# Performance work log

Measured on AMD Instinct MI355X. Metric: run time of the kernel, lower is better.

## Reference

```python
import jax, jax.numpy as jnp
import numpy as np

B, NPG, D, E = 64, 1024, 128, 524288
N = B * NPG
K1, K2, K3 = 820, 656, 525  # ceil(0.8*1024), ceil(0.8*820), ceil(0.8*656)
VOCAB = 100000
EPS = 1e-5


def setup_inputs() -> dict:
    key = jax.random.key(0)
    ks = jax.random.split(key, 16)
    epg = E // B
    off = jnp.repeat(jnp.arange(B, dtype=jnp.int32) * NPG, epg)
    src = jax.random.randint(ks[0], (E,), 0, NPG, dtype=jnp.int32) + off
    dst = jax.random.randint(ks[1], (E,), 0, NPG, dtype=jnp.int32) + off
    edge_index = jnp.stack([src, dst])  # [2, E], within-graph edges
    node_idx = jax.random.randint(ks[2], (N, 1), 0, VOCAB, dtype=jnp.int32)
    def lin(k, o, i):
        return jax.random.normal(k, (o, i), jnp.float32) / np.sqrt(i).astype(np.float32)
    return dict(
        node_idx=node_idx, edge_index=edge_index,
        emb=jax.random.normal(ks[3], (VOCAB, D), jnp.float32),
        w1l=lin(ks[4], 128, D), b1l=jnp.zeros(128, jnp.float32), w1r=lin(ks[5], 128, D),
        pool_w=jax.random.normal(ks[6], (128,), jnp.float32) / np.float32(np.sqrt(128)),
        w2l=lin(ks[7], 128, 128), b2l=jnp.zeros(128, jnp.float32), w2r=lin(ks[8], 128, 128),
        fc1_w=lin(ks[9], 128, 256), fc1_b=jnp.zeros(128, jnp.float32),
        bn1_g=jnp.ones(128, jnp.float32), bn1_b=jnp.zeros(128, jnp.float32),
        fc2_w=lin(ks[10], 64, 128), fc2_b=jnp.zeros(64, jnp.float32),
        bn2_g=jnp.ones(64, jnp.float32), bn2_b=jnp.zeros(64, jnp.float32),
        lin_w=lin(ks[11], 1, 64), lin_b=jnp.zeros(1, jnp.float32),
    )


def _sage(x, src, dst, em, wl, bl, wr):
    # PyG SAGEConv: lin_l(mean_{j->i} x_j) + lin_r(x_i); em masks dropped edges
    n = x.shape[0]
    s = jax.ops.segment_sum(x[src] * em[:, None], dst, num_segments=n)
    c = jax.ops.segment_sum(em, dst, num_segments=n)
    mean = s / jnp.maximum(c, 1.0)[:, None]
    return mean @ wl.T + bl + x @ wr.T


def _topk(x, src, dst, em, w, k):
    # PyG TopKPooling: score = x.w/||w||, per-graph top-k, gate by tanh(score)
    n = x.shape[0]
    npg = n // B
    score = (x @ w) / jnp.linalg.norm(w)
    vals, idx = jax.lax.top_k(score.reshape(B, npg), k)  # [B,k]
    perm = (idx + (jnp.arange(B, dtype=idx.dtype) * npg)[:, None]).reshape(-1)
    xn = x[perm] * jnp.tanh(vals).reshape(-1)[:, None]
    new_id = jnp.full((n,), -1, jnp.int32).at[perm].set(jnp.arange(B * k, dtype=jnp.int32))
    ns, nd = new_id[src], new_id[dst]
    em2 = em * (ns >= 0) * (nd >= 0)  # keep only edges with both endpoints kept
    return xn, jnp.maximum(ns, 0), jnp.maximum(nd, 0), em2


def _readout(x, k):
    # global_max_pool || global_mean_pool (graphs are contiguous, size k)
    xr = x.reshape(B, k, -1)
    return jnp.concatenate([xr.max(axis=1), xr.mean(axis=1)], axis=1)


def _bn(x, g, b):
    m = x.mean(0)
    v = jnp.mean((x - m) ** 2, axis=0)  # biased var, as in BatchNorm1d training
    return (x - m) / jnp.sqrt(v + EPS) * g + b


def reference(node_idx, edge_index, emb, w1l, b1l, w1r, pool_w,
              w2l, b2l, w2r, fc1_w, fc1_b, bn1_g, bn1_b,
              fc2_w, fc2_b, bn2_g, bn2_b, lin_w, lin_b):
    src, dst = edge_index[0], edge_index[1]
    em = jnp.ones((E,), jnp.float32)
    x = emb[node_idx[:, 0]]                                   # [N,128]
    x = jax.nn.relu(_sage(x, src, dst, em, w1l, b1l, w1r))
    x, src, dst, em = _topk(x, src, dst, em, pool_w, K1)
    x1 = _readout(x, K1)
    x = jax.nn.relu(_sage(x, src, dst, em, w2l, b2l, w2r))
    x, src, dst, em = _topk(x, src, dst, em, pool_w, K2)
    x2 = _readout(x, K2)
    x = jax.nn.relu(_sage(x, src, dst, em, w2l, b2l, w2r))
    x, src, dst, em = _topk(x, src, dst, em, pool_w, K3)
    x3 = _readout(x, K3)
    h = x1 + x2 + x3                                          # [B,256]
    h = jax.nn.relu(_bn(h @ fc1_w.T + fc1_b, bn1_g, bn1_b))
    h = jax.nn.relu(_bn(h @ fc2_w.T + fc2_b, bn2_g, bn2_b))
    # dropout is identity in eval mode
    return jax.nn.sigmoid(h @ lin_w.T + lin_b)[:, 0]          # [B]
```

## Files before the change

### kernel.cpp

```cpp
#include <hip/hip_runtime.h>
#include <hip/hip_bf16.h>
#include <cstdint>
#include <cstddef>

#define NGRAPH 64
#define NPG0   1024
#define NNODE  65536
#define NEDGE  524288
#define EPG    8192
#define DIM    128
#define RCHUNK 16

typedef __attribute__((ext_vector_type(8))) short short8v;
typedef __attribute__((ext_vector_type(4))) float f32x4;

__device__ __forceinline__ unsigned bf16rne(float f) {
  unsigned u = __float_as_uint(f);
  return (u + 0x7FFFu + ((u >> 16) & 1u)) >> 16;
}

__global__ __launch_bounds__(256) void k_gather(const float* __restrict__ emb,
    const int* __restrict__ nid, float* __restrict__ x)
{
  int tid = blockIdx.x * 256 + threadIdx.x;
  int i = tid >> 5, lane = tid & 31;
  int row = nid[i];
  ((float4*)(x + (size_t)i * DIM))[lane] =
      ((const float4*)(emb + (size_t)row * DIM))[lane];
}

__global__ __launch_bounds__(64) void k_norm(const float* __restrict__ pw,
    float* __restrict__ inv_norm)
{
  int t = threadIdx.x;
  float a = pw[t], b = pw[t + 64];
  float v = a * a + b * b;
  for (int off = 32; off; off >>= 1) v += __shfl_xor(v, off);
  if (t == 0) *inv_norm = 1.0f / sqrtf(v);
}

__global__ __launch_bounds__(256) void k_prep_wfrag(
    const float* __restrict__ w1l, const float* __restrict__ w1r,
    const float* __restrict__ w2l, const float* __restrict__ w2r,
    short* __restrict__ whiF, short* __restrict__ wloF)
{
  int id = blockIdx.x * 256 + threadIdx.x;
  int set = id >> 15;
  int r = id & 32767;
  int j  = r & 7;
  int l  = (r >> 3) & 63;
  int nt = (r >> 9) & 7;
  int kk = r >> 12;
  int k = kk * 32 + ((l >> 4) & 3) * 8 + j;
  int n = nt * 16 + (l & 15);
  const float* wl = set ? w2l : w1l;
  const float* wr = set ? w2r : w1r;
  float w = (k < 128) ? wl[n * 128 + k] : wr[n * 128 + (k - 128)];
  unsigned hb = bf16rne(w);
  float hif = __uint_as_float(hb << 16);
  unsigned lb = bf16rne(w - hif);
  whiF[id] = (short)hb;
  wloF[id] = (short)lb;
}

__global__ __launch_bounds__(1024) void k_csr0(const int* __restrict__ ei,
    int* __restrict__ off_g, int* __restrict__ elist_g, float* __restrict__ c_out)
{
  __shared__ int cnt[1024];
  __shared__ int cur[1024];
  __shared__ int wsum[16];
  const int t = threadIdx.x, g = blockIdx.x;
  const int nodeBase = g * NPG0;
  const int e0 = g * EPG;
  cnt[t] = 0;
  __syncthreads();
  int sv8[8], dl8[8];
  #pragma unroll
  for (int i = 0; i < 8; ++i) {
    int e = e0 + t + i * 1024;
    sv8[i] = ei[e];
    dl8[i] = ei[NEDGE + e] - nodeBase;
    atomicAdd(&cnt[dl8[i]], 1);
  }
  __syncthreads();
  const int lane = t & 63, w = t >> 6;
  int cv = cnt[t];
  int x = cv;
  #pragma unroll
  for (int off = 1; off < 64; off <<= 1) {
    int y = __shfl_up(x, off);
    if (lane >= off) x += y;
  }
  if (lane == 63) wsum[w] = x;
  __syncthreads();
  if (t < 16) {
    int v = wsum[t];
    #pragma unroll
    for (int off2 = 1; off2 < 16; off2 <<= 1) {
      int y = __shfl_up(v, off2);
      if (t >= off2) v += y;
    }
    wsum[t] = v;
  }
  __syncthreads();
  int incl = x + (w ? wsum[w - 1] : 0);
  int excl = incl - cv;
  cur[t] = excl;
  int* offp = off_g + g * 1025;
  offp[t] = excl;
  if (t == 1023) offp[1024] = incl;
  c_out[nodeBase + t] = (float)cv;
  __syncthreads();
  int* elp = elist_g + g * EPG;
  #pragma unroll
  for (int i = 0; i < 8; ++i) {
    int pos = atomicAdd(&cur[dl8[i]], 1);
    elp[pos] = sv8[i];
  }
}

__global__ __launch_bounds__(256) void k_gather_agg(
    const int* __restrict__ off_g, const int* __restrict__ elist_g,
    const float* __restrict__ x, float* __restrict__ s_out, int npg)
{
  const int g  = blockIdx.x & 63;
  const int sb = blockIdx.x >> 6;
  const int t = threadIdx.x;
  const int gr = t >> 5;
  const int l32 = t & 31;
  const int nq16 = (npg + 15) >> 4;
  const int vbase = sb * nq16;
  const int vend = min(npg, vbase + nq16);
  const int nodeBase = g * npg;
  const int* off = off_g + g * 1025;
  const int* el  = elist_g + g * EPG;
  const int cnt = vend - vbase;
  const int per = (cnt + 7) >> 3;
  int v0 = vbase + gr * per;
  int v1 = min(vend, v0 + per);
  for (int v = v0; v < v1; ++v) {
    int e   = off[v];
    int end = off[v + 1];
    float4 acc = {0.f, 0.f, 0.f, 0.f};
    for (; e + 4 <= end; e += 4) {
      int s0 = el[e], s1 = el[e + 1], s2 = el[e + 2], s3 = el[e + 3];
      float4 a0 = ((const float4*)(x + (size_t)s0 * DIM))[l32];
      float4 a1 = ((const float4*)(x + (size_t)s1 * DIM))[l32];
      float4 a2 = ((const float4*)(x + (size_t)s2 * DIM))[l32];
      float4 a3 = ((const float4*)(x + (size_t)s3 * DIM))[l32];
      acc.x += (a0.x + a1.x) + (a2.x + a3.x);
      acc.y += (a0.y + a1.y) + (a2.y + a3.y);
      acc.z += (a0.z + a1.z) + (a2.z + a3.z);
      acc.w += (a0.w + a1.w) + (a2.w + a3.w);
    }
    for (; e + 2 <= end; e += 2) {
      int s0 = el[e], s1 = el[e + 1];
      float4 a0 = ((const float4*)(x + (size_t)s0 * DIM))[l32];
      float4 a1 = ((const float4*)(x + (size_t)s1 * DIM))[l32];
      acc.x += a0.x + a1.x; acc.y += a0.y + a1.y;
      acc.z += a0.z + a1.z; acc.w += a0.w + a1.w;
    }
    if (e < end) {
      float4 a = ((const float4*)(x + (size_t)el[e] * DIM))[l32];
      acc.x += a.x; acc.y += a.y; acc.z += a.z; acc.w += a.w;
    }
    ((float4*)(s_out + (size_t)(nodeBase + v) * DIM))[l32] = acc;
  }
}

__global__ __launch_bounds__(256) void k_gemm_mfma(
    const float* __restrict__ x, float* __restrict__ s, const float* __restrict__ c,
    const short* __restrict__ whiF, const short* __restrict__ wloF,
    const float* __restrict__ bl, const float* __restrict__ pw,
    float* __restrict__ score)
{
  const int t = threadIdx.x;
  const int wv = t >> 6, l = t & 63;
  const int rowbase = blockIdx.x * 64 + wv * 16;
  const int lrow = l & 15, lk = l >> 4;
  const int row = rowbase + lrow;
  const float invc = 1.0f / fmaxf(c[row], 1.0f);
  f32x4 acc[8];
  #pragma unroll
  for (int nt = 0; nt < 8; ++nt) acc[nt] = (f32x4){0.f, 0.f, 0.f, 0.f};
  const float* srow = s + (size_t)row * DIM + lk * 8;
  const float* xrow = x + (size_t)row * DIM + lk * 8;
  const short8v* bh = (const short8v*)whiF;
  const short8v* bo = (const short8v*)wloF;

  #pragma unroll
  for (int kk = 0; kk < 8; ++kk) {
    const float* ap = (kk < 4) ? (srow + kk * 32) : (xrow + (kk - 4) * 32);
    float4 a0 = *(const float4*)ap;
    float4 a1 = *(const float4*)(ap + 4);
    float scl = (kk < 4) ? invc : 1.0f;
    float av[8] = { a0.x * scl, a0.y * scl, a0.z * scl, a0.w * scl,
                    a1.x * scl, a1.y * scl, a1.z * scl, a1.w * scl };
    short8v ahi, alo;
    #pragma unroll
    for (int j = 0; j < 8; ++j) {
      unsigned hb = bf16rne(av[j]);
      float hif = __uint_as_float(hb << 16);
      ahi[j] = (short)hb;
      alo[j] = (short)bf16rne(av[j] - hif);
    }
    #pragma unroll
    for (int nt = 0; nt < 8; ++nt) {
      int fi = (kk * 8 + nt) * 64 + l;
      short8v bhi = bh[fi];
      short8v blo = bo[fi];
      acc[nt] = __builtin_amdgcn_mfma_f32_16x16x32_bf16(ahi, bhi, acc[nt], 0, 0, 0);
      acc[nt] = __builtin_amdgcn_mfma_f32_16x16x32_bf16(alo, bhi, acc[nt], 0, 0, 0);
      acc[nt] = __builtin_amdgcn_mfma_f32_16x16x32_bf16(ahi, blo, acc[nt], 0, 0, 0);
    }
  }

  float sp0 = 0.f, sp1 = 0.f, sp2 = 0.f, sp3 = 0.f;
  const int mb = rowbase + lk * 4;
  #pragma unroll
  for (int nt = 0; nt < 8; ++nt) {
    int col = nt * 16 + lrow;
    float bb = bl[col], pv = pw[col];
    float h0 = fmaxf(acc[nt][0] + bb, 0.f);
    float h1 = fmaxf(acc[nt][1] + bb, 0.f);
    float h2 = fmaxf(acc[nt][2] + bb, 0.f);
    float h3 = fmaxf(acc[nt][3] + bb, 0.f);
    s[(size_t)(mb + 0) * DIM + col] = h0;
    s[(size_t)(mb + 1) * DIM + col] = h1;
    s[(size_t)(mb + 2) * DIM + col] = h2;
    s[(size_t)(mb + 3) * DIM + col] = h3;
    sp0 += h0 * pv; sp1 += h1 * pv; sp2 += h2 * pv; sp3 += h3 * pv;
  }
  #pragma unroll
  for (int off = 1; off <= 8; off <<= 1) {
    sp0 += __shfl_xor(sp0, off);
    sp1 += __shfl_xor(sp1, off);
    sp2 += __shfl_xor(sp2, off);
    sp3 += __shfl_xor(sp3, off);
  }
  if (lrow == 0) {
    score[mb + 0] = sp0;
    score[mb + 1] = sp1;
    score[mb + 2] = sp2;
    score[mb + 3] = sp3;
  }
}

__global__ __launch_bounds__(1024) void k_topk_fused(
    const float* __restrict__ score, const float* __restrict__ inv_norm_p,
    int npg, int k, int* __restrict__ sel_pos, float* __restrict__ sel_scale,
    int build_next, int write_eout,
    const int* __restrict__ ein_src, const int* __restrict__ ein_dst,
    int* __restrict__ eout_src, int* __restrict__ eout_dst,
    int* __restrict__ off_g, int* __restrict__ elist_g, float* __restrict__ c_out)
{
  __shared__ float key[1024];
  __shared__ int   idxs[1024];
  __shared__ int   nid[1024];
  __shared__ int   cnt[1024];
  __shared__ int   cur[1024];
  __shared__ int   wsum[16];
  const int t = threadIdx.x, g = blockIdx.x;
  const int base = g * npg;
  key[t] = (t < npg) ? score[base + t] : -3.402823466e38f;
  idxs[t] = t;
  nid[t] = -1;
  cnt[t] = 0;
  __syncthreads();
  for (int size = 2; size <= 1024; size <<= 1) {
    for (int stride = size >> 1; stride > 0; stride >>= 1) {
      int p = t ^ stride;
      if (p > t) {
        float ka = key[t], kb = key[p];
        int ia = idxs[t], ib = idxs[p];
        bool a_first = (ka > kb) || (ka == kb && ia < ib);
        bool desc = ((t & size) == 0);
        if (desc ? !a_first : a_first) {
          key[t] = kb; key[p] = ka; idxs[t] = ib; idxs[p] = ia;
        }
      }
      __syncthreads();
    }
  }
  if (t < k) {
    float inv = *inv_norm_p;
    int local = idxs[t];
    nid[local] = t;
    sel_pos[g * k + t] = base + local;
    sel_scale[g * k + t] = tanhf(key[t] * inv);
  }
  if (!build_next) return;
  __syncthreads();
  const int e0 = g * EPG;
  const int newBase = g * k;
  int lns[8], lnd[8];
  #pragma unroll
  for (int i = 0; i < 8; ++i) {
    int e = e0 + t + i * 1024;
    int sv = ein_src[e];
    int ns = -1, nd = -1;
    if (sv >= 0) {
      int dv = ein_dst[e];
      ns = nid[sv - base];
      nd = nid[dv - base];
      if (ns < 0 || nd < 0) ns = -1;
    }
    lns[i] = ns; lnd[i] = nd;
    if (write_eout) {
      eout_src[e] = (ns >= 0) ? (newBase + ns) : -1;
      eout_dst[e] = (ns >= 0) ? (newBase + nd) : -1;
    }
    if (ns >= 0) atomicAdd(&cnt[nd], 1);
  }
  __syncthreads();
  const int lane = t & 63, w = t >> 6;
  int cv = cnt[t];
  int x = cv;
  #pragma unroll
  for (int off = 1; off < 64; off <<= 1) {
    int y = __shfl_up(x, off);
    if (lane >= off) x += y;
  }
  if (lane == 63) wsum[w] = x;
  __syncthreads();
  if (t < 16) {
    int v = wsum[t];
    #pragma unroll
    for (int off2 = 1; off2 < 16; off2 <<= 1) {
      int y = __shfl_up(v, off2);
      if (t >= off2) v += y;
    }
    wsum[t] = v;
  }
  __syncthreads();
  int incl = x + (w ? wsum[w - 1] : 0);
  int excl = incl - cv;
  cur[t] = excl;
  off_g[g * 1025 + t] = excl;
  if (t < k) c_out[newBase + t] = (float)cv;
  __syncthreads();
  int* elp = elist_g + g * EPG;
  #pragma unroll
  for (int i = 0; i < 8; ++i) {
    if (lns[i] >= 0) {
      int pos = atomicAdd(&cur[lnd[i]], 1);
      elp[pos] = newBase + lns[i];
    }
  }
}

__global__ __launch_bounds__(256) void k_pool_part(const float* __restrict__ h,
    const int* __restrict__ sel_pos, const float* __restrict__ sel_scale, int k,
    float* __restrict__ xo, float* __restrict__ pmax, float* __restrict__ psum)
{
  __shared__ float4 smx[256], ssm[256];
  const int b  = blockIdx.x >> 4;
  const int ch = blockIdx.x & (RCHUNK - 1);
  const int rpc = (k + RCHUNK - 1) / RCHUNK;
  const int r0 = ch * rpc;
  const int r1 = min(k, r0 + rpc);
  const int d4  = threadIdx.x & 31;
  const int sub = threadIdx.x >> 5;
  const float NEG = -3.402823466e38f;
  float4 mx = {NEG, NEG, NEG, NEG};
  float4 sm = {0.f, 0.f, 0.f, 0.f};
  for (int r = r0 + sub; r < r1; r += 8) {
    int j = b * k + r;
    float scv = sel_scale[j];
    float4 v = ((const float4*)(h + (size_t)sel_pos[j] * DIM))[d4];
    v.x *= scv; v.y *= scv; v.z *= scv; v.w *= scv;
    ((float4*)(xo + (size_t)j * DIM))[d4] = v;
    mx.x = fmaxf(mx.x, v.x); mx.y = fmaxf(mx.y, v.y);
    mx.z = fmaxf(mx.z, v.z); mx.w = fmaxf(mx.w, v.w);
    sm.x += v.x; sm.y += v.y; sm.z += v.z; sm.w += v.w;
  }
  smx[threadIdx.x] = mx; ssm[threadIdx.x] = sm;
  __syncthreads();
  if (sub < 4) {
    #pragma unroll
    for (int step = 4; step >= 1; step >>= 1) {
      if (sub < step) {
        float4 m2 = smx[(sub + step) * 32 + d4];
        float4 s2 = ssm[(sub + step) * 32 + d4];
        mx = smx[sub * 32 + d4]; sm = ssm[sub * 32 + d4];
        mx.x = fmaxf(mx.x, m2.x); mx.y = fmaxf(mx.y, m2.y);
        mx.z = fmaxf(mx.z, m2.z); mx.w = fmaxf(mx.w, m2.w);
        sm.x += s2.x; sm.y += s2.y; sm.z += s2.z; sm.w += s2.w;
        smx[sub * 32 + d4] = mx; ssm[sub * 32 + d4] = sm;
      }
      __syncthreads();
    }
  }
  if (sub == 0) {
    int o = (b * RCHUNK + ch) * 32 + d4;
    ((float4*)pmax)[o] = smx[d4];
    ((float4*)psum)[o] = ssm[d4];
  }
}

__global__ __launch_bounds__(128) void k_readout_final(const float* __restrict__ pmax,
    const float* __restrict__ psum, int k, float* __restrict__ rdT, int add)
{
  int b = blockIdx.x, d = threadIdx.x;
  float mx = -3.402823466e38f, sm = 0.f;
  #pragma unroll
  for (int c = 0; c < RCHUNK; ++c) {
    int o = (b * RCHUNK + c) * 128 + d;
    mx = fmaxf(mx, pmax[o]);
    sm += psum[o];
  }
  float mean = sm / (float)k;
  int omx = d * 64 + b;
  int omn = (128 + d) * 64 + b;
  if (add) { rdT[omx] += mx; rdT[omn] += mean; }
  else     { rdT[omx]  = mx; rdT[omn]  = mean; }
}

__global__ __launch_bounds__(512) void k_mlp_fc1(const float* __restrict__ rdT,
    const float* __restrict__ fc1_w, const float* __restrict__ fc1_b,
    const float* __restrict__ g1, const float* __restrict__ be1,
    float* __restrict__ y1n)
{
  __shared__ float W[8 * 256];
  __shared__ float R[256 * 64];
  const int t = threadIdx.x, b = blockIdx.x;
  ((float4*)W)[t] = ((const float4*)(fc1_w + (size_t)b * 8 * 256))[t];
  #pragma unroll
  for (int i = 0; i < 8; ++i)
    ((float4*)R)[t + i * 512] = ((const float4*)rdT)[t + i * 512];
  __syncthreads();
  const int g = t & 63, w = t >> 6;
  const float* wrow = W + w * 256;
  float acc = 0.f;
  #pragma unroll 4
  for (int k = 0; k < 256; ++k) acc += R[k * 64 + g] * wrow[k];
  int f = b * 8 + w;
  float y = acc + fc1_b[f];
  float s = y, s2 = y * y;
  #pragma unroll
  for (int off = 32; off; off >>= 1) {
    s  += __shfl_xor(s,  off);
    s2 += __shfl_xor(s2, off);
  }
  float mu = s * 0.015625f;
  float var = s2 * 0.015625f - mu * mu;
  float inv = 1.0f / sqrtf(var + 1e-5f);
  y1n[f * 64 + g] = fmaxf((y - mu) * inv * g1[f] + be1[f], 0.f);
}

__global__ __launch_bounds__(1024) void k_mlp_rest(const float* __restrict__ y1n,
    const float* __restrict__ fc2_w, const float* __restrict__ fc2_b,
    const float* __restrict__ g2, const float* __restrict__ be2,
    const float* __restrict__ lin_w, const float* __restrict__ lin_b,
    float* __restrict__ out)
{
  __shared__ float W2[64 * 128];
  __shared__ float Y[128 * 64];
  __shared__ float part[16 * 64];
  const int t = threadIdx.x;
  #pragma unroll
  for (int i = 0; i < 2; ++i) {
    ((float4*)W2)[t + i * 1024] = ((const float4*)fc2_w)[t + i * 1024];
    ((float4*)Y) [t + i * 1024] = ((const float4*)y1n)[t + i * 1024];
  }
  __syncthreads();
  const int g = t & 63, w = t >> 6;
  float acc2[4] = {0.f, 0.f, 0.f, 0.f};
  const float* w20 = W2 + (w * 4 + 0) * 128;
  const float* w21 = W2 + (w * 4 + 1) * 128;
  const float* w22 = W2 + (w * 4 + 2) * 128;
  const float* w23 = W2 + (w * 4 + 3) * 128;
  #pragma unroll 4
  for (int k = 0; k < 128; ++k) {
    float yv = Y[k * 64 + g];
    acc2[0] += yv * w20[k];
    acc2[1] += yv * w21[k];
    acc2[2] += yv * w22[k];
    acc2[3] += yv * w23[k];
  }
  float pp = 0.f;
  #pragma unroll
  for (int j = 0; j < 4; ++j) {
    int m = w * 4 + j;
    float y = acc2[j] + fc2_b[m];
    float s = y, s2 = y * y;
    #pragma unroll
    for (int off = 32; off; off >>= 1) {
      s  += __shfl_xor(s,  off);
      s2 += __shfl_xor(s2, off);
    }
    float mu = s * 0.015625f;
    float var = s2 * 0.015625f - mu * mu;
    float inv = 1.0f / sqrtf(var + 1e-5f);
    float yn = fmaxf((y - mu) * inv * g2[m] + be2[m], 0.f);
    pp += yn * lin_w[m];
  }
  part[w * 64 + g] = pp;
  __syncthreads();
  if (w == 0) {
    float a = lin_b[0];
    #pragma unroll
    for (int c = 0; c < 16; ++c) a += part[c * 64 + g];
    out[g] = 1.0f / (1.0f + expf(-a));
  }
}

extern "C" void kernel_launch(void* const* d_in, const int* in_sizes, int n_in,
                              void* d_out, int out_size, void* d_ws, size_t ws_size,
                              hipStream_t stream) {
  const int*   node_idx = (const int*)  d_in[0];
  const int*   edge_idx = (const int*)  d_in[1];
  const float* emb      = (const float*)d_in[2];
  const float* w1l      = (const float*)d_in[3];
  const float* b1l      = (const float*)d_in[4];
  const float* w1r      = (const float*)d_in[5];
  const float* pool_w   = (const float*)d_in[6];
  const float* w2l      = (const float*)d_in[7];
  const float* b2l      = (const float*)d_in[8];
  const float* w2r      = (const float*)d_in[9];
  const float* fc1_w    = (const float*)d_in[10];
  const float* fc1_b    = (const float*)d_in[11];
  const float* bn1_g    = (const float*)d_in[12];
  const float* bn1_b    = (const float*)d_in[13];
  const float* fc2_w    = (const float*)d_in[14];
  const float* fc2_b    = (const float*)d_in[15];
  const float* bn2_g    = (const float*)d_in[16];
  const float* bn2_b    = (const float*)d_in[17];
  const float* lin_w    = (const float*)d_in[18];
  const float* lin_b    = (const float*)d_in[19];
  float* out = (float*)d_out;

  char* p = (char*)d_ws;
  auto alloc = [&](size_t bytes) -> void* {
    void* r = (void*)p;
    p += (bytes + 255) & ~(size_t)255;
    return r;
  };
  float* x_cur     = (float*)alloc((size_t)NNODE * DIM * 4);
  float* s_buf     = (float*)alloc((size_t)NNODE * DIM * 4);
  float* c_buf     = (float*)alloc((size_t)NNODE * 4);
  float* score     = (float*)alloc((size_t)NNODE * 4);
  int*   sel_pos   = (int*)  alloc((size_t)NGRAPH * 820 * 4);
  float* sel_scale = (float*)alloc((size_t)NGRAPH * 820 * 4);
  int*   src_cur   = (int*)  alloc((size_t)NEDGE * 4);
  int*   dst_cur   = (int*)  alloc((size_t)NEDGE * 4);
  int*   off_g     = (int*)  alloc((size_t)NGRAPH * 1025 * 4);
  int*   elist_g   = (int*)  alloc((size_t)NGRAPH * EPG * 4);
  float* rdT       = (float*)alloc((size_t)256 * 64 * 4);
  short* whiF      = (short*)alloc((size_t)2 * 32768 * 2);
  short* wloF      = (short*)alloc((size_t)2 * 32768 * 2);
  float* y1n       = (float*)alloc((size_t)128 * 64 * 4);
  float* pmax      = (float*)alloc((size_t)NGRAPH * RCHUNK * 128 * 4);
  float* psum      = (float*)alloc((size_t)NGRAPH * RCHUNK * 128 * 4);
  float* inv_norm  = (float*)alloc(256);

  k_gather<<<NNODE * 32 / 256, 256, 0, stream>>>(emb, node_idx, x_cur);
  k_norm<<<1, 64, 0, stream>>>(pool_w, inv_norm);
  k_prep_wfrag<<<256, 256, 0, stream>>>(w1l, w1r, w2l, w2r, whiF, wloF);
  k_csr0<<<NGRAPH, 1024, 0, stream>>>(edge_idx, off_g, elist_g, c_buf);

  const int Ks[3] = {820, 656, 525};
  int npg = NPG0;
  for (int stage = 0; stage < 3; ++stage) {
    const short* whi_s = whiF + (stage ? 32768 : 0);
    const short* wlo_s = wloF + (stage ? 32768 : 0);
    const float* bl    = stage ? b2l : b1l;
    int n = NGRAPH * npg;
    int k = Ks[stage];

    k_gather_agg<<<16 * NGRAPH, 256, 0, stream>>>(off_g, elist_g, x_cur, s_buf, npg);
    k_gemm_mfma<<<n / 64, 256, 0, stream>>>(x_cur, s_buf, c_buf, whi_s, wlo_s,
                                            bl, pool_w, score);
    const int* ein_s = (stage == 0) ? edge_idx          : src_cur;
    const int* ein_d = (stage == 0) ? (edge_idx + NEDGE) : dst_cur;
    k_topk_fused<<<NGRAPH, 1024, 0, stream>>>(score, inv_norm, npg, k,
        sel_pos, sel_scale,
        (stage < 2) ? 1 : 0, (stage == 0) ? 1 : 0,
        ein_s, ein_d, src_cur, dst_cur,
        off_g, elist_g, c_buf);
    k_pool_part<<<NGRAPH * RCHUNK, 256, 0, stream>>>(s_buf, sel_pos, sel_scale, k,
                                                     x_cur, pmax, psum);
    k_readout_final<<<NGRAPH, 128, 0, stream>>>(pmax, psum, k, rdT, stage == 0 ? 0 : 1);
    npg = k;
  }

  k_mlp_fc1<<<16, 512, 0, stream>>>(rdT, fc1_w, fc1_b, bn1_g, bn1_b, y1n);
  k_mlp_rest<<<1, 1024, 0, stream>>>(y1n, fc2_w, fc2_b, bn2_g, bn2_b,
                                     lin_w, lin_b, out);
}
```

Measured before the change: 296.7 us.

## Fuse neighbor mean aggregation into MFMA GEMM via shared-memory tile

Merges the neighbour-gather aggregation kernel and the MFMA SAGE GEMM into one kernel. Each block aggregates 64 nodes of one graph into LDS together with their edge counts, then runs the split-bf16 MFMA GEMM straight from LDS. This drops the global write and re-read of the aggregated buffer and one launch per stage. In exchange it uses 32KB of LDS per block, which may lower occupancy for the latency-bound gather. It also handles stage sizes that are not multiples of 64 through per-graph slices with bounds checks.

```diff
diff --git a/kernel.cpp b/kernel.cpp
--- a/kernel.cpp
+++ b/kernel.cpp
@@ -119,83 +119,93 @@
   }
 }
 
-__global__ __launch_bounds__(256) void k_gather_agg(
+__global__ __launch_bounds__(256) void k_agg_gemm(
     const int* __restrict__ off_g, const int* __restrict__ elist_g,
-    const float* __restrict__ x, float* __restrict__ s_out, int npg)
-{
-  const int g  = blockIdx.x & 63;
-  const int sb = blockIdx.x >> 6;
-  const int t = threadIdx.x;
-  const int gr = t >> 5;
-  const int l32 = t & 31;
-  const int nq16 = (npg + 15) >> 4;
-  const int vbase = sb * nq16;
-  const int vend = min(npg, vbase + nq16);
-  const int nodeBase = g * npg;
-  const int* off = off_g + g * 1025;
-  const int* el  = elist_g + g * EPG;
-  const int cnt = vend - vbase;
-  const int per = (cnt + 7) >> 3;
-  int v0 = vbase + gr * per;
-  int v1 = min(vend, v0 + per);
-  for (int v = v0; v < v1; ++v) {
-    int e   = off[v];
-    int end = off[v + 1];
-    float4 acc = {0.f, 0.f, 0.f, 0.f};
-    for (; e + 4 <= end; e += 4) {
-      int s0 = el[e], s1 = el[e + 1], s2 = el[e + 2], s3 = el[e + 3];
-      float4 a0 = ((const float4*)(x + (size_t)s0 * DIM))[l32];
-      float4 a1 = ((const float4*)(x + (size_t)s1 * DIM))[l32];
-      float4 a2 = ((const float4*)(x + (size_t)s2 * DIM))[l32];
-      float4 a3 = ((const float4*)(x + (size_t)s3 * DIM))[l32];
-      acc.x += (a0.x + a1.x) + (a2.x + a3.x);
-      acc.y += (a0.y + a1.y) + (a2.y + a3.y);
-      acc.z += (a0.z + a1.z) + (a2.z + a3.z);
-      acc.w += (a0.w + a1.w) + (a2.w + a3.w);
-    }
-    for (; e + 2 <= end; e += 2) {
-      int s0 = el[e], s1 = el[e + 1];
-      float4 a0 = ((const float4*)(x + (size_t)s0 * DIM))[l32];
-      float4 a1 = ((const float4*)(x + (size_t)s1 * DIM))[l32];
-      acc.x += a0.x + a1.x; acc.y += a0.y + a1.y;
-      acc.z += a0.z + a1.z; acc.w += a0.w + a1.w;
-    }
-    if (e < end) {
-      float4 a = ((const float4*)(x + (size_t)el[e] * DIM))[l32];
-      acc.x += a.x; acc.y += a.y; acc.z += a.z; acc.w += a.w;
-    }
-    ((float4*)(s_out + (size_t)(nodeBase + v) * DIM))[l32] = acc;
-  }
-}
-
-__global__ __launch_bounds__(256) void k_gemm_mfma(
-    const float* __restrict__ x, float* __restrict__ s, const float* __restrict__ c,
+    const float* __restrict__ x, float* __restrict__ h_out,
     const short* __restrict__ whiF, const short* __restrict__ wloF,
     const float* __restrict__ bl, const float* __restrict__ pw,
-    float* __restrict__ score)
-{
+    float* __restrict__ score, int npg)
+{
+  __shared__ float sA[64 * 128];
+  __shared__ float cntA[64];
+  const int g     = blockIdx.x & 63;
+  const int slice = blockIdx.x >> 6;
+  const int nodeBase = g * npg;
+  const int vbase = slice * 64;
   const int t = threadIdx.x;
+
+  {
+    const int gr = t >> 5, l32 = t & 31;
+    const int* off = off_g + g * 1025;
+    const int* el  = elist_g + g * EPG;
+    #pragma unroll
+    for (int i = 0; i < 8; ++i) {
+      int vb = gr * 8 + i;
+      int v = vbase + vb;
+      float4 acc = {0.f, 0.f, 0.f, 0.f};
+      int cn = 0;
+      if (v < npg) {
+        int e = off[v], end = off[v + 1];
+        cn = end - e;
+        for (; e + 4 <= end; e += 4) {
+          int s0 = el[e], s1 = el[e + 1], s2 = el[e + 2], s3 = el[e + 3];
+          float4 a0 = ((const float4*)(x + (size_t)s0 * DIM))[l32];
+          float4 a1 = ((const float4*)(x + (size_t)s1 * DIM))[l32];
+          float4 a2 = ((const float4*)(x + (size_t)s2 * DIM))[l32];
+          float4 a3 = ((const float4*)(x + (size_t)s3 * DIM))[l32];
+          acc.x += (a0.x + a1.x) + (a2.x + a3.x);
+          acc.y += (a0.y + a1.y) + (a2.y + a3.y);
+          acc.z += (a0.z + a1.z) + (a2.z + a3.z);
+          acc.w += (a0.w + a1.w) + (a2.w + a3.w);
+        }
+        for (; e + 2 <= end; e += 2) {
+          int s0 = el[e], s1 = el[e + 1];
+          float4 a0 = ((const float4*)(x + (size_t)s0 * DIM))[l32];
+          float4 a1 = ((const float4*)(x + (size_t)s1 * DIM))[l32];
+          acc.x += a0.x + a1.x; acc.y += a0.y + a1.y;
+          acc.z += a0.z + a1.z; acc.w += a0.w + a1.w;
+        }
+        if (e < end) {
+          float4 a = ((const float4*)(x + (size_t)el[e] * DIM))[l32];
+          acc.x += a.x; acc.y += a.y; acc.z += a.z; acc.w += a.w;
+        }
+      }
+      ((float4*)(sA + vb * 128))[l32] = acc;
+      if (l32 == 0) cntA[vb] = (float)cn;
+    }
+  }
+  __syncthreads();
+
   const int wv = t >> 6, l = t & 63;
-  const int rowbase = blockIdx.x * 64 + wv * 16;
   const int lrow = l & 15, lk = l >> 4;
-  const int row = rowbase + lrow;
-  const float invc = 1.0f / fmaxf(c[row], 1.0f);
+  const int rb = wv * 16;
+  const int rowb = rb + lrow;
+  const int rowg = nodeBase + min(vbase + rowb, npg - 1);
+  const float invc = 1.0f / fmaxf(cntA[rowb], 1.0f);
   f32x4 acc[8];
   #pragma unroll
   for (int nt = 0; nt < 8; ++nt) acc[nt] = (f32x4){0.f, 0.f, 0.f, 0.f};
-  const float* srow = s + (size_t)row * DIM + lk * 8;
-  const float* xrow = x + (size_t)row * DIM + lk * 8;
+  const float* srow = sA + rowb * 128 + lk * 8;
+  const float* xrow = x + (size_t)rowg * DIM + lk * 8;
   const short8v* bh = (const short8v*)whiF;
   const short8v* bo = (const short8v*)wloF;
 
   #pragma unroll
   for (int kk = 0; kk < 8; ++kk) {
-    const float* ap = (kk < 4) ? (srow + kk * 32) : (xrow + (kk - 4) * 32);
-    float4 a0 = *(const float4*)ap;
-    float4 a1 = *(const float4*)(ap + 4);
-    float scl = (kk < 4) ? invc : 1.0f;
-    float av[8] = { a0.x * scl, a0.y * scl, a0.z * scl, a0.w * scl,
-                    a1.x * scl, a1.y * scl, a1.z * scl, a1.w * scl };
+    float av[8];
+    if (kk < 4) {
+      float4 a0 = *(const float4*)(srow + kk * 32);
+      float4 a1 = *(const float4*)(srow + kk * 32 + 4);
+      av[0] = a0.x * invc; av[1] = a0.y * invc;
+      av[2] = a0.z * invc; av[3] = a0.w * invc;
+      av[4] = a1.x * invc; av[5] = a1.y * invc;
+      av[6] = a1.z * invc; av[7] = a1.w * invc;
+    } else {
+      float4 a0 = *(const float4*)(xrow + (kk - 4) * 32);
+      float4 a1 = *(const float4*)(xrow + (kk - 4) * 32 + 4);
+      av[0] = a0.x; av[1] = a0.y; av[2] = a0.z; av[3] = a0.w;
+      av[4] = a1.x; av[5] = a1.y; av[6] = a1.z; av[7] = a1.w;
+    }
     short8v ahi, alo;
     #pragma unroll
     for (int j = 0; j < 8; ++j) {
@@ -216,7 +226,7 @@
   }
 
   float sp0 = 0.f, sp1 = 0.f, sp2 = 0.f, sp3 = 0.f;
-  const int mb = rowbase + lk * 4;
+  const int mbv = vbase + rb + lk * 4;
   #pragma unroll
   for (int nt = 0; nt < 8; ++nt) {
     int col = nt * 16 + lrow;
@@ -225,10 +235,10 @@
     float h1 = fmaxf(acc[nt][1] + bb, 0.f);
     float h2 = fmaxf(acc[nt][2] + bb, 0.f);
     float h3 = fmaxf(acc[nt][3] + bb, 0.f);
-    s[(size_t)(mb + 0) * DIM + col] = h0;
-    s[(size_t)(mb + 1) * DIM + col] = h1;
-    s[(size_t)(mb + 2) * DIM + col] = h2;
-    s[(size_t)(mb + 3) * DIM + col] = h3;
+    if (mbv + 0 < npg) h_out[(size_t)(nodeBase + mbv + 0) * DIM + col] = h0;
+    if (mbv + 1 < npg) h_out[(size_t)(nodeBase + mbv + 1) * DIM + col] = h1;
+    if (mbv + 2 < npg) h_out[(size_t)(nodeBase + mbv + 2) * DIM + col] = h2;
+    if (mbv + 3 < npg) h_out[(size_t)(nodeBase + mbv + 3) * DIM + col] = h3;
     sp0 += h0 * pv; sp1 += h1 * pv; sp2 += h2 * pv; sp3 += h3 * pv;
   }
   #pragma unroll
@@ -239,10 +249,10 @@
     sp3 += __shfl_xor(sp3, off);
   }
   if (lrow == 0) {
-    score[mb + 0] = sp0;
-    score[mb + 1] = sp1;
-    score[mb + 2] = sp2;
-    score[mb + 3] = sp3;
+    if (mbv + 0 < npg) score[nodeBase + mbv + 0] = sp0;
+    if (mbv + 1 < npg) score[nodeBase + mbv + 1] = sp1;
+    if (mbv + 2 < npg) score[nodeBase + mbv + 2] = sp2;
+    if (mbv + 3 < npg) score[nodeBase + mbv + 3] = sp3;
   }
 }
 
@@ -565,12 +575,12 @@
     const short* whi_s = whiF + (stage ? 32768 : 0);
     const short* wlo_s = wloF + (stage ? 32768 : 0);
     const float* bl    = stage ? b2l : b1l;
-    int n = NGRAPH * npg;
     int k = Ks[stage];
-
-    k_gather_agg<<<16 * NGRAPH, 256, 0, stream>>>(off_g, elist_g, x_cur, s_buf, npg);
-    k_gemm_mfma<<<n / 64, 256, 0, stream>>>(x_cur, s_buf, c_buf, whi_s, wlo_s,
-                                            bl, pool_w, score);
+    int slices = (npg + 63) >> 6;
+
+    k_agg_gemm<<<slices * 64, 256, 0, stream>>>(off_g, elist_g, x_cur, s_buf,
+                                                whi_s, wlo_s, bl, pool_w,
+                                                score, npg);
     const int* ein_s = (stage == 0) ? edge_idx          : src_cur;
     const int* ein_d = (stage == 0) ? (edge_idx + NEDGE) : dst_cur;
     k_topk_fused<<<NGRAPH, 1024, 0, stream>>>(score, inv_norm, npg, k,
```

Result: faster. 277.3 us (-6.5%).
